# Kernel optimization log

Measured on AMD Instinct MI355X. Metric: run time of the kernel, lower is better.

The kernel has to match this reference:

```python
import jax, jax.numpy as jnp
import numpy as np

B, T = 32, 2048
Q_DIM, K_DIM, V_DIM, A_DIM = 512, 512, 512, 128
TEMP = 1.0


def setup_inputs() -> dict:
    key = jax.random.key(0)
    ks = jax.random.split(key, 8)
    return {
        "query": jax.random.normal(ks[0], (B, Q_DIM), dtype=jnp.float32),
        "keys": jax.random.normal(ks[1], (B, T, K_DIM), dtype=jnp.float32),
        "values": jax.random.normal(ks[2], (B, T, V_DIM), dtype=jnp.float32),
        "prev_attention_weights": jax.random.uniform(ks[3], (B, T), dtype=jnp.float32),
        "mask": jnp.ones((B, T), dtype=jnp.int32),
        # learned params (nn.Linear weight is [out,in]; store as [in,out])
        "Wq": jax.random.normal(ks[4], (Q_DIM, A_DIM), dtype=jnp.float32) * 0.02,
        "Wk": jax.random.normal(ks[5], (K_DIM, A_DIM), dtype=jnp.float32) * 0.02,
        "We": jax.random.normal(ks[6], (A_DIM, 1), dtype=jnp.float32) * 0.02,
    }


def reference(query, keys, values, prev_attention_weights, mask, Wq, Wk, We):
    # additive attention energies
    qp = query @ Wq                                   # [B, A]
    kp = jnp.einsum('btk,ka->bta', keys, Wk)          # [B, T, A]
    energy = jnp.squeeze(jnp.tanh(kp + qp[:, None, :]) @ We, -1)  # [B, T]
    energy = jnp.where(mask == 0, -jnp.inf, energy)
    raw = jax.nn.softmax(energy / TEMP, axis=1)
    # forward attention: fw[0]=raw[0]; fw[t]=(prev[t-1]+prev[t])*raw[t] for t>=1
    prev = prev_attention_weights
    prev_shift = jnp.pad(prev[:, :-1], ((0, 0), (1, 0)))  # prev[t-1], zero at t=0
    fw = raw * (prev + prev_shift)
    fw = fw.at[:, 0].set(raw[:, 0])
    fw = fw / (fw.sum(axis=1, keepdims=True) + 1e-8)
    context = jnp.einsum('bt,btd->bd', fw, values)    # [B, V_DIM]
    return context, fw
```

## Files before the change

### kernel.cpp

```cpp
#include <hip/hip_runtime.h>
#include <cstdint>
#include <cstddef>


#define T_ 2048
#define KD 512
#define AD 128

typedef __attribute__((ext_vector_type(8))) short bf16x8;
typedef __attribute__((ext_vector_type(4))) float f32x4;

__device__ __forceinline__ unsigned pack2bf(float a, float b) {
    unsigned ua = __float_as_uint(a), ub = __float_as_uint(b);
    ua += 0x7FFFu + ((ua >> 16) & 1u);
    ub += 0x7FFFu + ((ub >> 16) & 1u);
    return (ua >> 16) | (ub & 0xFFFF0000u);
}

__global__ __launch_bounds__(256) void prep_kernel(
    const float* __restrict__ query, const float* __restrict__ Wq,
    const float* __restrict__ Wk, float* __restrict__ qp,
    unsigned short* __restrict__ WkT)
{
    __shared__ float sq[128];
    const int tid = threadIdx.x;
    if (blockIdx.x < 32) {
        const int b = blockIdx.x;
        const int a = tid & 127, half = tid >> 7;
        const float* q = query + (size_t)b * KD + half * 256;
        const float* w = Wq + (size_t)(half * 256) * AD + a;
        float s0 = 0.f, s1 = 0.f, s2 = 0.f, s3 = 0.f;
        #pragma unroll 4
        for (int k = 0; k < 256; k += 4) {
            s0 += q[k + 0] * w[(size_t)(k + 0) * AD];
            s1 += q[k + 1] * w[(size_t)(k + 1) * AD];
            s2 += q[k + 2] * w[(size_t)(k + 2) * AD];
            s3 += q[k + 3] * w[(size_t)(k + 3) * AD];
        }
        float s = (s0 + s1) + (s2 + s3);
        if (half == 0) sq[a] = s;
        __syncthreads();
        if (half == 1) qp[(size_t)b * AD + a] = sq[a] + s;
    } else {
        const int blk2 = blockIdx.x - 32;
        const int n = tid & 127, kr = tid >> 7;
        #pragma unroll
        for (int kk = 0; kk < 8; kk++) {
            int k = blk2 * 16 + kr * 8 + kk;
            float v = Wk[(size_t)k * AD + n];
            unsigned u = __float_as_uint(v);
            u += 0x7FFFu + ((u >> 16) & 1u);
            WkT[(size_t)n * KD + k] = (unsigned short)(u >> 16);
        }
    }
}

__global__ __launch_bounds__(256, 2) void energy_kernel(
    const float* __restrict__ keys, const unsigned short* __restrict__ WkT,
    const float* __restrict__ qp, const float* __restrict__ We,
    float* __restrict__ energy)
{
    __shared__ __align__(16) unsigned short sA[128 * 40];
    __shared__ __align__(16) unsigned short sB[128 * 40];
    const int tid = threadIdx.x;
    const int m0 = blockIdx.x * 128;
    const int b = m0 >> 11;

    const int row = tid >> 1, half = tid & 1;
    const float* gA = keys + (size_t)(m0 + row) * KD + half * 16;
    const unsigned short* gB = WkT + (size_t)row * KD + half * 16;
    unsigned short* dA = &sA[row * 40 + half * 16];
    unsigned short* dB = &sB[row * 40 + half * 16];

    const int lane = tid & 63, wv = tid >> 6;
    const int lr = lane & 15, quad = lane >> 4;

    f32x4 acc[2][8];
    #pragma unroll
    for (int mt = 0; mt < 2; mt++)
        #pragma unroll
        for (int nt = 0; nt < 8; nt++)
            acc[mt][nt] = (f32x4){0.f, 0.f, 0.f, 0.f};

    for (int k0 = 0; k0 < KD; k0 += 32) {
        float4 f0 = *(const float4*)(gA + k0 + 0);
        float4 f1 = *(const float4*)(gA + k0 + 4);
        float4 f2 = *(const float4*)(gA + k0 + 8);
        float4 f3 = *(const float4*)(gA + k0 + 12);
        uint4 pa0, pa1;
        pa0.x = pack2bf(f0.x, f0.y); pa0.y = pack2bf(f0.z, f0.w);
        pa0.z = pack2bf(f1.x, f1.y); pa0.w = pack2bf(f1.z, f1.w);
        pa1.x = pack2bf(f2.x, f2.y); pa1.y = pack2bf(f2.z, f2.w);
        pa1.z = pack2bf(f3.x, f3.y); pa1.w = pack2bf(f3.z, f3.w);
        uint4 b0 = *(const uint4*)(gB + k0);
        uint4 b1 = *(const uint4*)(gB + k0 + 8);
        ((uint4*)dA)[0] = pa0; ((uint4*)dA)[1] = pa1;
        ((uint4*)dB)[0] = b0;  ((uint4*)dB)[1] = b1;
        __syncthreads();

        bf16x8 af[2], bfm[8];
        #pragma unroll
        for (int mt = 0; mt < 2; mt++)
            af[mt] = *(const bf16x8*)&sA[(wv * 32 + mt * 16 + lr) * 40 + quad * 8];
        #pragma unroll
        for (int nt = 0; nt < 8; nt++)
            bfm[nt] = *(const bf16x8*)&sB[(nt * 16 + lr) * 40 + quad * 8];
        #pragma unroll
        for (int mt = 0; mt < 2; mt++)
            #pragma unroll
            for (int nt = 0; nt < 8; nt++)
                acc[mt][nt] = __builtin_amdgcn_mfma_f32_16x16x32_bf16(
                    af[mt], bfm[nt], acc[mt][nt], 0, 0, 0);
        __syncthreads();
    }

    float part[2][4] = {{0.f, 0.f, 0.f, 0.f}, {0.f, 0.f, 0.f, 0.f}};
    #pragma unroll
    for (int nt = 0; nt < 8; nt++) {
        int col = nt * 16 + lr;
        float we = We[col];
        float q  = qp[(size_t)b * AD + col];
        #pragma unroll
        for (int mt = 0; mt < 2; mt++)
            #pragma unroll
            for (int r = 0; r < 4; r++) {
                float x = acc[mt][nt][r] + q;
                float e2 = __expf(2.0f * x);
                float th = 1.0f - 2.0f / (e2 + 1.0f);
                part[mt][r] += we * th;
            }
    }
    #pragma unroll
    for (int mt = 0; mt < 2; mt++)
        #pragma unroll
        for (int r = 0; r < 4; r++) {
            float v = part[mt][r];
            v += __shfl_xor(v, 1); v += __shfl_xor(v, 2);
            v += __shfl_xor(v, 4); v += __shfl_xor(v, 8);
            if (lr == 0)
                energy[(size_t)m0 + wv * 32 + mt * 16 + quad * 4 + r] = v;
        }
}

__device__ __forceinline__ float block_red_max(float v, float* sred) {
    #pragma unroll
    for (int m = 1; m < 64; m <<= 1) v = fmaxf(v, __shfl_xor(v, m));
    if ((threadIdx.x & 63) == 0) sred[threadIdx.x >> 6] = v;
    __syncthreads();
    float r = fmaxf(fmaxf(sred[0], sred[1]), fmaxf(sred[2], sred[3]));
    __syncthreads();
    return r;
}
__device__ __forceinline__ float block_red_sum(float v, float* sred) {
    #pragma unroll
    for (int m = 1; m < 64; m <<= 1) v += __shfl_xor(v, m);
    if ((threadIdx.x & 63) == 0) sred[threadIdx.x >> 6] = v;
    __syncthreads();
    float r = (sred[0] + sred[1]) + (sred[2] + sred[3]);
    __syncthreads();
    return r;
}

__global__ __launch_bounds__(256) void softmax_fw_kernel(
    const float* __restrict__ prev, const int* __restrict__ mask,
    float* __restrict__ fw)
{
    __shared__ float sred[4];
    const int b = blockIdx.x, tid = threadIdx.x;
    const size_t base = (size_t)b * T_;
    float e[8];
    #pragma unroll
    for (int i = 0; i < 8; i++) {
        int t = tid + 256 * i;
        float ev = fw[base + t];
        if (mask[base + t] == 0) ev = -__builtin_inff();
        e[i] = ev;
    }
    float mx = e[0];
    #pragma unroll
    for (int i = 1; i < 8; i++) mx = fmaxf(mx, e[i]);
    mx = block_red_max(mx, sred);

    float ex[8]; float s = 0.f;
    #pragma unroll
    for (int i = 0; i < 8; i++) { ex[i] = __expf(e[i] - mx); s += ex[i]; }
    s = block_red_sum(s, sred);
    const float invS = 1.0f / s;

    float fwv[8]; float s2 = 0.f;
    #pragma unroll
    for (int i = 0; i < 8; i++) {
        int t = tid + 256 * i;
        float pv = prev[base + t];
        float pm = (t == 0) ? 0.f : prev[base + t - 1];
        float r = ex[i] * invS;
        fwv[i] = (t == 0) ? r : r * (pv + pm);
        s2 += fwv[i];
    }
    s2 = block_red_sum(s2, sred);
    const float invD = 1.0f / (s2 + 1e-8f);
    #pragma unroll
    for (int i = 0; i < 8; i++)
        fw[base + tid + 256 * i] = fwv[i] * invD;
}

__global__ __launch_bounds__(256) void ctx_partial_kernel(
    const float* __restrict__ values, const float* __restrict__ fw,
    float* __restrict__ part)
{
    __shared__ float sfw[128];
    __shared__ float4 sacc[128];
    const int b = blockIdx.x >> 4, ts = blockIdx.x & 15;
    const int tid = threadIdx.x;
    const int t0 = ts * 128;
    if (tid < 128) sfw[tid] = fw[(size_t)b * T_ + t0 + tid];
    __syncthreads();
    const int d4 = tid & 127, tp = tid >> 7;
    const float4* vp = (const float4*)values + ((size_t)b * T_ + t0 + tp) * 128 + d4;
    float4 acc = {0.f, 0.f, 0.f, 0.f};
    #pragma unroll 4
    for (int i = 0; i < 64; i++) {
        float f = sfw[tp + 2 * i];
        float4 v = vp[(size_t)i * 256];
        acc.x += f * v.x; acc.y += f * v.y; acc.z += f * v.z; acc.w += f * v.w;
    }
    if (tp) sacc[d4] = acc;
    __syncthreads();
    if (!tp) {
        float4 o = sacc[d4];
        o.x += acc.x; o.y += acc.y; o.z += acc.z; o.w += acc.w;
        ((float4*)part)[(size_t)blockIdx.x * 128 + d4] = o;
    }
}

__global__ __launch_bounds__(256) void ctx_reduce_kernel(
    const float* __restrict__ part, float* __restrict__ ctx)
{
    const int idx = blockIdx.x * 256 + threadIdx.x;
    const int b = idx >> 9, d = idx & 511;
    float s = 0.f;
    #pragma unroll
    for (int ts = 0; ts < 16; ts++)
        s += part[((size_t)(b * 16 + ts)) * 512 + d];
    ctx[idx] = s;
}

extern "C" void kernel_launch(void* const* d_in, const int* in_sizes, int n_in,
                              void* d_out, int out_size, void* d_ws, size_t ws_size,
                              hipStream_t stream) {
    const float* query  = (const float*)d_in[0];
    const float* keys   = (const float*)d_in[1];
    const float* values = (const float*)d_in[2];
    const float* prev   = (const float*)d_in[3];
    const int*   mask   = (const int*)d_in[4];
    const float* Wq     = (const float*)d_in[5];
    const float* Wk     = (const float*)d_in[6];
    const float* We     = (const float*)d_in[7];

    float* ctx = (float*)d_out;
    float* fw  = ctx + 32 * 512;

    float* wsf = (float*)d_ws;
    float* qp   = wsf;
    float* part = wsf + 4096;
    unsigned short* WkT = (unsigned short*)(wsf + 4096 + 262144);

    prep_kernel<<<dim3(64), dim3(256), 0, stream>>>(query, Wq, Wk, qp, WkT);
    energy_kernel<<<dim3(512), dim3(256), 0, stream>>>(keys, WkT, qp, We, fw);
    softmax_fw_kernel<<<dim3(32), dim3(256), 0, stream>>>(prev, mask, fw);
    ctx_partial_kernel<<<dim3(512), dim3(256), 0, stream>>>(values, fw, part);
    ctx_reduce_kernel<<<dim3(64), dim3(256), 0, stream>>>(part, ctx);
}
```

Baseline: 311.7 us.

## Fuse softmax/forward-attention into context partial kernel with redundant per-block softmax

```diff
diff --git a/kernel.cpp b/kernel.cpp
--- a/kernel.cpp
+++ b/kernel.cpp
@@ -161,18 +161,23 @@
     return r;
 }
 
-__global__ __launch_bounds__(256) void softmax_fw_kernel(
-    const float* __restrict__ prev, const int* __restrict__ mask,
-    float* __restrict__ fw)
+__global__ __launch_bounds__(256) void ctx_fused_kernel(
+    const float* __restrict__ energy, const float* __restrict__ prev,
+    const int* __restrict__ mask, const float* __restrict__ values,
+    float* __restrict__ fw, float* __restrict__ part)
 {
     __shared__ float sred[4];
-    const int b = blockIdx.x, tid = threadIdx.x;
+    __shared__ float sfw[2048];
+    __shared__ float4 sacc[128];
+    const int b = blockIdx.x >> 4, ts = blockIdx.x & 15;
+    const int tid = threadIdx.x;
     const size_t base = (size_t)b * T_;
+
     float e[8];
     #pragma unroll
     for (int i = 0; i < 8; i++) {
         int t = tid + 256 * i;
-        float ev = fw[base + t];
+        float ev = energy[base + t];
         if (mask[base + t] == 0) ev = -__builtin_inff();
         e[i] = ev;
     }
@@ -201,26 +206,19 @@
     const float invD = 1.0f / (s2 + 1e-8f);
     #pragma unroll
     for (int i = 0; i < 8; i++)
-        fw[base + tid + 256 * i] = fwv[i] * invD;
-}
-
-__global__ __launch_bounds__(256) void ctx_partial_kernel(
-    const float* __restrict__ values, const float* __restrict__ fw,
-    float* __restrict__ part)
-{
-    __shared__ float sfw[128];
-    __shared__ float4 sacc[128];
-    const int b = blockIdx.x >> 4, ts = blockIdx.x & 15;
-    const int tid = threadIdx.x;
+        sfw[tid + 256 * i] = fwv[i] * invD;
+    __syncthreads();
+
     const int t0 = ts * 128;
-    if (tid < 128) sfw[tid] = fw[(size_t)b * T_ + t0 + tid];
-    __syncthreads();
+    if (tid < 128) fw[base + t0 + tid] = sfw[t0 + tid];
+
     const int d4 = tid & 127, tp = tid >> 7;
+    const float* sf = &sfw[t0];
     const float4* vp = (const float4*)values + ((size_t)b * T_ + t0 + tp) * 128 + d4;
     float4 acc = {0.f, 0.f, 0.f, 0.f};
-    #pragma unroll 4
+    #pragma unroll 8
     for (int i = 0; i < 64; i++) {
-        float f = sfw[tp + 2 * i];
+        float f = sf[tp + 2 * i];
         float4 v = vp[(size_t)i * 256];
         acc.x += f * v.x; acc.y += f * v.y; acc.z += f * v.z; acc.w += f * v.w;
     }
@@ -261,13 +259,13 @@
     float* fw  = ctx + 32 * 512;
 
     float* wsf = (float*)d_ws;
-    float* qp   = wsf;
-    float* part = wsf + 4096;
-    unsigned short* WkT = (unsigned short*)(wsf + 4096 + 262144);
+    float* qp     = wsf;
+    float* part   = wsf + 4096;
+    float* energy = wsf + 4096 + 262144;
+    unsigned short* WkT = (unsigned short*)(wsf + 4096 + 262144 + 65536);
 
     prep_kernel<<<dim3(64), dim3(256), 0, stream>>>(query, Wq, Wk, qp, WkT);
-    energy_kernel<<<dim3(512), dim3(256), 0, stream>>>(keys, WkT, qp, We, fw);
-    softmax_fw_kernel<<<dim3(32), dim3(256), 0, stream>>>(prev, mask, fw);
-    ctx_partial_kernel<<<dim3(512), dim3(256), 0, stream>>>(values, fw, part);
+    energy_kernel<<<dim3(512), dim3(256), 0, stream>>>(keys, WkT, qp, We, energy);
+    ctx_fused_kernel<<<dim3(512), dim3(256), 0, stream>>>(energy, prev, mask, values, fw, part);
     ctx_reduce_kernel<<<dim3(64), dim3(256), 0, stream>>>(part, ctx);
 }
```

New measurement: 310.9 us. Within noise of the previous version (-0.3%).
